# Performance work log

Hardware: AMD Instinct MI355X
Metric: run time of the kernel (lower is better)

## Reference

```python
import jax, jax.numpy as jnp
import numpy as np

EPS = 1e-5

def mean_std_norm(x):
    # instance norm without affine: per-(B,C) mean/std over spatial dims
    mean = jnp.mean(x, axis=(2, 3), keepdims=True)
    var = jnp.var(x, axis=(2, 3), keepdims=True)
    return (x - mean) / jnp.sqrt(var + EPS)

def conv1x1(x, w, b):
    # x: [B,C,H,W], w: [O,C], b: [O]
    return jnp.einsum('oc,bchw->bohw', w, x) + b[None, :, None, None]

def setup_inputs() -> dict:
    key = jax.random.key(0)
    ks = jax.random.split(key, 9)
    C = 512
    s = 1.0 / np.sqrt(C)
    inp = {
        'content_feat': jax.random.normal(ks[0], (4, C, 64, 64), dtype=jnp.float32),
        'f_w': jax.random.normal(ks[1], (C, C), dtype=jnp.float32) * s,
        'f_b': jnp.zeros((C,), dtype=jnp.float32),
        'g_w': jax.random.normal(ks[2], (C, C), dtype=jnp.float32) * s,
        'g_b': jnp.zeros((C,), dtype=jnp.float32),
        'h_w': jax.random.normal(ks[3], (C, C), dtype=jnp.float32) * s,
        'h_b': jnp.zeros((C,), dtype=jnp.float32),
        'o_w': jax.random.normal(ks[4], (C, C), dtype=jnp.float32) * s,
        'o_b': jnp.zeros((C,), dtype=jnp.float32),
    }
    return inp

def reference(content_feat, f_w, f_b, g_w, g_b, h_w, h_b, o_w, o_b):
    B, C, H, W = content_feat.shape
    HW = H * W
    norm = mean_std_norm(content_feat)
    # f(norm) -> [B, HW, C]; g(norm) -> [B, C, HW]
    F_Fc = conv1x1(norm, f_w, f_b).reshape(B, C, HW).transpose(0, 2, 1)
    G_Fs = conv1x1(norm, g_w, g_b).reshape(B, C, HW)
    energy = jnp.einsum('bnc,bcm->bnm', F_Fc, G_Fs)  # [B, HW, HW]
    attention = jax.nn.softmax(energy, axis=-1)
    H_Fs = conv1x1(content_feat, h_w, h_b).reshape(B, C, HW)
    # out = H_Fs @ attention^T : out[b,c,m] = sum_n H_Fs[b,c,n] * att[b,m,n]
    out = jnp.einsum('bcn,bmn->bcm', H_Fs, attention).reshape(B, C, H, W)
    out = conv1x1(out, o_w, o_b)
    return out + content_feat
```

## Files before the change

kernel.cpp:

```cpp
#include <hip/hip_runtime.h>


typedef __bf16 bf16_t;
typedef _Float16 f16_t;
typedef _Float16 f16x8 __attribute__((ext_vector_type(8)));
typedef float f32x4 __attribute__((ext_vector_type(4)));

#define LOG2E 1.44269504088896340736f

__device__ __forceinline__ void gload16(const void* g, void* l) {
  __builtin_amdgcn_global_load_lds(
      (const __attribute__((address_space(1))) void*)g,
      (__attribute__((address_space(3))) void*)l, 16, 0, 0);
}

__global__ void __launch_bounds__(256) stats_k(const float* __restrict__ x,
                                               float* __restrict__ mu,
                                               float* __restrict__ rs) {
  const int bc = blockIdx.x;
  const float4* row = (const float4*)(x + (size_t)bc * 4096);
  float s = 0.f, ss = 0.f;
  for (int i = threadIdx.x; i < 1024; i += 256) {
    float4 v = row[i];
    s += v.x + v.y + v.z + v.w;
    ss += v.x * v.x + v.y * v.y + v.z * v.z + v.w * v.w;
  }
#pragma unroll
  for (int o = 32; o >= 1; o >>= 1) {
    s += __shfl_down(s, o);
    ss += __shfl_down(ss, o);
  }
  __shared__ float as_[4], ass_[4];
  const int w = threadIdx.x >> 6;
  if ((threadIdx.x & 63) == 0) { as_[w] = s; ass_[w] = ss; }
  __syncthreads();
  if (threadIdx.x == 0) {
    float st = as_[0] + as_[1] + as_[2] + as_[3];
    float sst = ass_[0] + ass_[1] + ass_[2] + ass_[3];
    float m = st * (1.f / 4096.f);
    float var = sst * (1.f / 4096.f) - m * m;
    mu[bc] = m;
    rs[bc] = rsqrtf(var + 1e-5f);
  }
}

__global__ void __launch_bounds__(256) wcast2_k(const float* __restrict__ a,
                                                const float* __restrict__ b,
                                                f16_t* __restrict__ dst) {
  const int i = blockIdx.x * 256 + threadIdx.x;
  const int which = i >> 16;
  const int off = i & 65535;
  const float* s = which ? b : a;
  const float4 v = ((const float4*)s)[off];
  alignas(8) f16_t r[4];
  r[0] = (f16_t)v.x; r[1] = (f16_t)v.y; r[2] = (f16_t)v.z; r[3] = (f16_t)v.w;
  *(uint2*)(dst + ((size_t)which << 18) + (size_t)off * 4) = *(const uint2*)r;
}

__global__ void __launch_bounds__(256) mt_k(const float* __restrict__ fw,
                                            const float* __restrict__ gw,
                                            f16_t* __restrict__ Mh) {
  __shared__ float Fs[32][64];
  __shared__ float Gs[32][64];
  const int t = threadIdx.x;
  const int it = blockIdx.x, jt = blockIdx.y;
  float acc[16];
#pragma unroll
  for (int i = 0; i < 16; ++i) acc[i] = 0.f;
  const int jl = t >> 2, ib = (t & 3) * 16;
  const int lr = t >> 4, lc4 = (t & 15) * 4;
  for (int cc = 0; cc < 16; ++cc) {
    __syncthreads();
#pragma unroll
    for (int rep = 0; rep < 2; ++rep) {
      const int r = lr + rep * 16;
      *(float4*)&Fs[r][lc4] = *(const float4*)(fw + (size_t)(cc * 32 + r) * 512 + it * 64 + lc4);
      *(float4*)&Gs[r][lc4] = *(const float4*)(gw + (size_t)(cc * 32 + r) * 512 + jt * 64 + lc4);
    }
    __syncthreads();
#pragma unroll
    for (int c = 0; c < 32; ++c) {
      const float gv = Gs[c][jl];
#pragma unroll
      for (int ii = 0; ii < 16; ++ii) acc[ii] += gv * Fs[c][ib + ii];
    }
  }
  alignas(16) f16_t hi[16];
#pragma unroll
  for (int ii = 0; ii < 16; ++ii) hi[ii] = (f16_t)acc[ii];
  const size_t o = (size_t)(jt * 64 + jl) * 512 + it * 64 + ib;
  *(uint4*)(Mh + o) = *(const uint4*)hi;
  *(uint4*)(Mh + o + 8) = *(const uint4*)(hi + 8);
}

__global__ void __launch_bounds__(256) v_k(const float* __restrict__ gw,
                                           const float* __restrict__ fb,
                                           float* __restrict__ v) {
  const int j = blockIdx.x * 256 + threadIdx.x;
  float s = 0.f;
  for (int c = 0; c < 512; ++c) s += gw[(size_t)c * 512 + j] * fb[c];
  v[j] = s;
}

__global__ void __launch_bounds__(256) u_k(const float* __restrict__ v,
                                           const f16_t* __restrict__ xf,
                                           float* __restrict__ u) {
  const int w = threadIdx.x >> 6, lane = threadIdx.x & 63;
  const int m = blockIdx.x * 4 + w;
  const int b = blockIdx.y;
  const size_t o = ((size_t)b * 4096 + m) * 512 + lane * 8;
  const f16x8 vh = *(const f16x8*)(xf + o);
  const float4 v0 = *(const float4*)(v + lane * 8);
  const float4 v1 = *(const float4*)(v + lane * 8 + 4);
  float s = 0.f;
  const float* vp = &v0.x;
#pragma unroll
  for (int e = 0; e < 4; ++e) s += (float)vh[e] * vp[e];
  const float* vq = &v1.x;
#pragma unroll
  for (int e = 0; e < 4; ++e) s += (float)vh[4 + e] * vq[e];
#pragma unroll
  for (int o2 = 32; o2 >= 1; o2 >>= 1) s += __shfl_down(s, o2);
  if (lane == 0) u[(size_t)b * 4096 + m] = s;
}

__global__ void __launch_bounds__(256) normt_k(const float* __restrict__ x,
                                               const float* __restrict__ mu,
                                               const float* __restrict__ rs,
                                               f16_t* __restrict__ xf,
                                               f16_t* __restrict__ xc) {
  __shared__ float tile[64][65];
  const int t = threadIdx.x;
  const int nt = blockIdx.x, ct = blockIdx.y, b = blockIdx.z;
  const float* src = x + ((size_t)b * 512 + ct * 64) * 4096 + nt * 64;
  {
    const int r = t >> 4, cq = (t & 15) * 4;
#pragma unroll
    for (int it = 0; it < 4; ++it) {
      const int rr = r + it * 16;
      const float4 v = *(const float4*)(src + (size_t)rr * 4096 + cq);
      tile[rr][cq] = v.x; tile[rr][cq + 1] = v.y;
      tile[rr][cq + 2] = v.z; tile[rr][cq + 3] = v.w;
    }
  }
  __syncthreads();
  const int n = t & 63, ch = t >> 6;
  alignas(16) f16_t vf[16], vc[16];
#pragma unroll
  for (int i = 0; i < 16; ++i) {
    const int c = ch * 16 + i;
    const float v = tile[c][n];
    const int gc = b * 512 + ct * 64 + c;
    vc[i] = (f16_t)v;
    vf[i] = (f16_t)((v - mu[gc]) * rs[gc]);
  }
  const size_t o = ((size_t)b * 4096 + nt * 64 + n) * 512 + ct * 64 + ch * 16;
  *(uint4*)(xf + o) = *(const uint4*)vf;
  *(uint4*)(xf + o + 8) = *(const uint4*)(vf + 8);
  *(uint4*)(xc + o) = *(const uint4*)vc;
  *(uint4*)(xc + o + 8) = *(const uint4*)(vc + 8);
}

template <typename OT, int BIAS, bool RESID>
__global__ void __launch_bounds__(256) gemm_k(const f16_t* __restrict__ A,
                                              const f16_t* __restrict__ Bt,
                                              OT* __restrict__ C,
                                              const float* __restrict__ biasM,
                                              const float* __restrict__ biasN,
                                              const float* __restrict__ resid,
                                              long sAb, long sBb, long sCb, int ldC) {
  __shared__ alignas(16) f16_t As[2][128 * 64];
  __shared__ alignas(16) f16_t Bs[2][128 * 64];
  const int t = threadIdx.x;
  const int lane = t & 63;
  const int w = t >> 6;
  const int wr = w >> 1, wc = w & 1;
  const int l15 = lane & 15, lg = lane >> 4;
  const int b = blockIdx.z;
  const int m0 = blockIdx.y * 128, n0 = blockIdx.x * 128;
  const f16_t* Ab = A + (size_t)sAb * b + (size_t)m0 * 512;
  const f16_t* Bb = Bt + (size_t)sBb * b + (size_t)n0 * 512;
  const int srow = t >> 3;
  const int slot = t & 7;

  auto gstage = [&](int pb_, int ks_) {
#pragma unroll
    for (int r_ = 0; r_ < 4; ++r_) {
      const int rr_ = r_ * 32 + srow;
      const size_t go_ = (size_t)rr_ * 512 + ks_ * 64 + ((slot ^ (rr_ & 7)) * 8);
      gload16(Ab + go_, (char*)As[pb_] + r_ * 4096 + w * 1024);
      gload16(Bb + go_, (char*)Bs[pb_] + r_ * 4096 + w * 1024);
    }
  };

  const f32x4 z4 = {0.f, 0.f, 0.f, 0.f};
  f32x4 acc[4][4];
#pragma unroll
  for (int i = 0; i < 4; ++i)
#pragma unroll
    for (int j = 0; j < 4; ++j) acc[i][j] = z4;

  gstage(0, 0);
  __syncthreads();
  for (int ks = 0; ks < 8; ++ks) {
    const int pb = ks & 1;
    if (ks < 7) gstage(pb ^ 1, ks + 1);
#pragma unroll
    for (int kk = 0; kk < 2; ++kk) {
      f16x8 af[4], bfr[4];
#pragma unroll
      for (int i = 0; i < 4; ++i) {
        const int ra = wr * 64 + i * 16 + l15;
        af[i] = *(const f16x8*)((const char*)As[pb] + ra * 128 + (((kk * 4 + lg) ^ (ra & 7)) * 16));
        const int rb = wc * 64 + i * 16 + l15;
        bfr[i] = *(const f16x8*)((const char*)Bs[pb] + rb * 128 + (((kk * 4 + lg) ^ (rb & 7)) * 16));
      }
#pragma unroll
      for (int i = 0; i < 4; ++i)
#pragma unroll
        for (int j = 0; j < 4; ++j)
          acc[i][j] = __builtin_amdgcn_mfma_f32_16x16x32_f16(af[i], bfr[j], acc[i][j], 0, 0, 0);
    }
    __syncthreads();
  }
  OT* Cb = C + (size_t)sCb * b;
#pragma unroll
  for (int i = 0; i < 4; ++i) {
#pragma unroll
    for (int j = 0; j < 4; ++j) {
      const int n = n0 + wc * 64 + j * 16 + l15;
      float bn = 0.f;
      if (BIAS == 2) bn = biasN[n];
#pragma unroll
      for (int r = 0; r < 4; ++r) {
        const int m = m0 + wr * 64 + i * 16 + lg * 4 + r;
        float v = acc[i][j][r] + bn;
        if (BIAS == 1) v += biasM[m];
        if (RESID) v += resid[(size_t)sCb * b + (size_t)m * ldC + n];
        Cb[(size_t)m * ldC + n] = (OT)v;
      }
    }
  }
}

__global__ void __launch_bounds__(512, 1) flash_k(const f16_t* __restrict__ Z,
                                                  const f16_t* __restrict__ X,
                                                  const float* __restrict__ u,
                                                  const f16_t* __restrict__ Hv,
                                                  f16_t* __restrict__ Oat_t) {
  __shared__ alignas(16) f16_t K[2][64 * 256];
  __shared__ alignas(16) f16_t P[64 * 72];
  __shared__ float redm[4][2][16];
  __shared__ float reds[4][2][16];
  __shared__ float alds[64];
  __shared__ float llds[64];

  const int t = threadIdx.x;
  const int lane = t & 63;
  const int w = t >> 6;
  const int wq = w & 3, wk = w >> 2;
  const int l15 = lane & 15, lg = lane >> 4;
  const int bid = blockIdx.x;
  const int xcd = bid & 7;
  const int b = xcd >> 1;
  const int q0 = ((xcd & 1) * 32 + (bid >> 3)) * 64;

  const f16_t* Kb = X + (size_t)b * 4096 * 512;
  const f16_t* Vb = Hv + (size_t)b * 512 * 4096;
  const float* ub = u + (size_t)b * 4096;

  const int srow = w * 2 + (lane >> 5);
  const int slot32 = lane & 31;

  auto stagek = [&](int pb_, int kt_, int hf_) {
    const int k0_ = kt_ * 64;
#pragma unroll
    for (int r_ = 0; r_ < 4; ++r_) {
      const int row_ = r_ * 16 + srow;
      const size_t go_ = (size_t)(k0_ + row_) * 512 + hf_ * 256 + ((slot32 ^ (row_ & 7)) * 8);
      gload16(Kb + go_, (char*)K[pb_] + r_ * 8192 + w * 1024);
    }
  };

#define QKHALF(PB, HF)                                                                        \
  do {                                                                                        \
    _Pragma("unroll") for (int cwl_ = 0; cwl_ < 8; ++cwl_) {                                  \
      const f16x8 qf_ = qf[(HF) * 8 + cwl_];                                                  \
      _Pragma("unroll") for (int mf_ = 0; mf_ < 2; ++mf_) {                                   \
        const int key_ = 32 * wk + 16 * mf_ + l15;                                            \
        const int so_ = ((cwl_ * 4 + lg) ^ (key_ & 7)) * 16;                                  \
        const f16x8 kf_ = *(const f16x8*)((const char*)K[PB] + key_ * 512 + so_);             \
        sacc[mf_] = __builtin_amdgcn_mfma_f32_16x16x32_f16(kf_, qf_, sacc[mf_], 0, 0, 0);     \
      }                                                                                       \
    }                                                                                         \
  } while (0)

  f16x8 qf[16];
  {
    const size_t qo = ((size_t)b * 4096 + q0 + 16 * wq + l15) * 512 + lg * 8;
#pragma unroll
    for (int cw = 0; cw < 16; ++cw) qf[cw] = *(const f16x8*)(Z + qo + cw * 32);
  }
  stagek(0, 0, 0);

  const f32x4 z4 = {0.f, 0.f, 0.f, 0.f};
  f32x4 oacc[4][4];
#pragma unroll
  for (int i = 0; i < 4; ++i)
#pragma unroll
    for (int j = 0; j < 4; ++j) oacc[i][j] = z4;
  float m_run = -3.0e38f, l_run = 0.f;
  const int qrow = 16 * wq + l15;

  __syncthreads();

  for (int kt = 0; kt < 64; ++kt) {
    const int k0 = kt * 64;
    f32x4 sacc[2] = {z4, z4};
    const float4 u0 = *(const float4*)(ub + k0 + 32 * wk + 4 * lg);
    const float4 u1 = *(const float4*)(ub + k0 + 32 * wk + 16 + 4 * lg);
    stagek(1, kt, 1);
    QKHALF(0, 0);
    __syncthreads();
    if (kt < 63) stagek(0, kt + 1, 0);
    f16x8 vpre[4][2];
#pragma unroll
    for (int ct = 0; ct < 4; ++ct) {
      const int c = 64 * w + 16 * ct + l15;
#pragma unroll
      for (int kk = 0; kk < 2; ++kk)
        vpre[ct][kk] = *(const f16x8*)(Vb + (size_t)c * 4096 + k0 + kk * 32 + lg * 8);
    }
    QKHALF(1, 1);
    float pm = -3.0e38f;
    {
      const float* up0 = &u0.x;
      const float* up1 = &u1.x;
#pragma unroll
      for (int j = 0; j < 4; ++j) {
        sacc[0][j] += up0[j];
        sacc[1][j] += up1[j];
        pm = fmaxf(pm, fmaxf(sacc[0][j], sacc[1][j]));
      }
    }
    pm = fmaxf(pm, __shfl_xor(pm, 16));
    pm = fmaxf(pm, __shfl_xor(pm, 32));
    if (lane < 16) redm[wq][wk][lane] = pm;
    __syncthreads();
    const float m_tile = fmaxf(pm, redm[wq][wk ^ 1][l15]);
    float alpha;
    if (m_tile > m_run + 8.f) {
      alpha = exp2f((m_run - m_tile) * LOG2E);
      m_run = m_tile;
    } else {
      alpha = 1.f;
    }
    float ps = 0.f;
    {
      alignas(8) f16_t pk[4];
#pragma unroll
      for (int mf = 0; mf < 2; ++mf) {
#pragma unroll
        for (int j = 0; j < 4; ++j) {
          const float p = exp2f((sacc[mf][j] - m_run) * LOG2E);
          ps += p;
          pk[j] = (f16_t)p;
        }
        *(uint2*)((char*)P + qrow * 144 + 64 * wk + 32 * mf + 8 * lg) = *(const uint2*)pk;
      }
    }
    ps += __shfl_xor(ps, 16);
    ps += __shfl_xor(ps, 32);
    if (lane < 16) {
      reds[wq][wk][lane] = ps;
      if (wk == 0) alds[16 * wq + lane] = alpha;
    }
    __syncthreads();
    const float s_tile = reds[wq][0][l15] + reds[wq][1][l15];
    l_run = l_run * alpha + s_tile;
    float aq[4];
#pragma unroll
    for (int qt = 0; qt < 4; ++qt) aq[qt] = alds[16 * qt + l15];
    const bool need = (aq[0] != 1.f) || (aq[1] != 1.f) || (aq[2] != 1.f) || (aq[3] != 1.f);
    if (__any(need)) {
#pragma unroll
      for (int ct = 0; ct < 4; ++ct)
#pragma unroll
        for (int qt = 0; qt < 4; ++qt) oacc[ct][qt] *= aq[qt];
    }
#pragma unroll
    for (int kk = 0; kk < 2; ++kk) {
      f16x8 bp[4];
#pragma unroll
      for (int qt = 0; qt < 4; ++qt) {
        const int q = 16 * qt + l15;
        bp[qt] = *(const f16x8*)((const char*)P + q * 144 + kk * 64 + lg * 16);
      }
#pragma unroll
      for (int ct = 0; ct < 4; ++ct)
#pragma unroll
        for (int qt = 0; qt < 4; ++qt)
          oacc[ct][qt] =
              __builtin_amdgcn_mfma_f32_16x16x32_f16(vpre[ct][kk], bp[qt], oacc[ct][qt], 0, 0, 0);
    }
  }
#undef QKHALF
  if (wk == 0 && lane < 16) llds[16 * wq + lane] = l_run;
  __syncthreads();
  float inv[4];
#pragma unroll
  for (int qt = 0; qt < 4; ++qt) inv[qt] = 1.f / llds[16 * qt + l15];
#pragma unroll
  for (int ct = 0; ct < 4; ++ct)
#pragma unroll
    for (int qt = 0; qt < 4; ++qt) {
      alignas(8) f16_t o4[4];
#pragma unroll
      for (int j = 0; j < 4; ++j) o4[j] = (f16_t)(oacc[ct][qt][j] * inv[qt]);
      *(uint2*)(Oat_t + ((size_t)b * 4096 + q0 + 16 * qt + l15) * 512 + 64 * w + 16 * ct + 4 * lg) =
          *(const uint2*)o4;
    }
}

extern "C" void kernel_launch(void* const* d_in, const int* in_sizes, int n_in,
                              void* d_out, int out_size, void* d_ws, size_t ws_size,
                              hipStream_t stream) {
  const float* x = (const float*)d_in[0];
  const float* fw = (const float*)d_in[1];
  const float* fb = (const float*)d_in[2];
  const float* gw = (const float*)d_in[3];
  const float* gb = (const float*)d_in[4];
  const float* hw = (const float*)d_in[5];
  const float* hb = (const float*)d_in[6];
  const float* ow = (const float*)d_in[7];
  const float* ob = (const float*)d_in[8];
  float* out = (float*)d_out;
  (void)gb;

  const size_t BIG = (size_t)4 * 4096 * 512 * sizeof(f16_t);
  char* p = (char*)d_ws;
  float* mu = (float*)p; p += 2048 * sizeof(float);
  float* rs = (float*)p; p += 2048 * sizeof(float);
  float* vv = (float*)p; p += 512 * sizeof(float);
  float* uu = (float*)p; p += (size_t)4 * 4096 * sizeof(float);
  f16_t* w2 = (f16_t*)p; p += (size_t)2 * 512 * 512 * sizeof(f16_t);
  f16_t* Mh = (f16_t*)p; p += (size_t)512 * 512 * sizeof(f16_t);
  f16_t* xf = (f16_t*)p; p += BIG;
  f16_t* xc = (f16_t*)p; p += BIG;
  f16_t* Zf = (f16_t*)p; p += BIG;
  f16_t* Hv = (f16_t*)p; p += BIG;
  f16_t* Oat_t = xc;

  f16_t* whb = w2;
  f16_t* wob = w2 + 262144;

  const long sD = (long)4096 * 512;

  stats_k<<<2048, 256, 0, stream>>>(x, mu, rs);
  wcast2_k<<<512, 256, 0, stream>>>(hw, ow, w2);
  mt_k<<<dim3(8, 8), 256, 0, stream>>>(fw, gw, Mh);
  v_k<<<2, 256, 0, stream>>>(gw, fb, vv);
  normt_k<<<dim3(64, 8, 4), 256, 0, stream>>>(x, mu, rs, xf, xc);
  u_k<<<dim3(1024, 4), 256, 0, stream>>>(vv, xf, uu);
  gemm_k<f16_t, 0, false><<<dim3(4, 32, 4), 256, 0, stream>>>(
      xf, Mh, Zf, nullptr, nullptr, nullptr, sD, 0, sD, 512);
  gemm_k<f16_t, 1, false><<<dim3(32, 4, 4), 256, 0, stream>>>(
      whb, xc, Hv, hb, nullptr, nullptr, 0, sD, sD, 4096);
  flash_k<<<256, 512, 0, stream>>>(Zf, xf, uu, Hv, Oat_t);
  gemm_k<float, 1, true><<<dim3(32, 4, 4), 256, 0, stream>>>(
      wob, Oat_t, out, ob, nullptr, x, 0, sD, sD, 4096);

  (void)in_sizes; (void)n_in; (void)out_size; (void)ws_size;
}
```

Measured before the change: 373.4 us.

## Process two key tiles per softmax step and split QK accumulators

The flash attention loop now handles 128 keys per iteration: two 64-key tiles of QK^T are computed before a single max/sum reduction and rescale. This halves the softmax reduction and barrier overhead per key. The QK MFMA chain is also split into even and odd accumulators to shorten dependency chains. The P buffer is widened to 128 columns, and register pressure rises from holding two V prefetch sets and four score tiles.

```diff
diff --git a/kernel.cpp b/kernel.cpp
--- a/kernel.cpp
+++ b/kernel.cpp
@@ -249,7 +249,7 @@
                                                   const f16_t* __restrict__ Hv,
                                                   f16_t* __restrict__ Oat_t) {
   __shared__ alignas(16) f16_t K[2][64 * 256];
-  __shared__ alignas(16) f16_t P[64 * 72];
+  __shared__ alignas(16) f16_t P[64 * 136];
   __shared__ float redm[4][2][16];
   __shared__ float reds[4][2][16];
   __shared__ float alds[64];
@@ -282,17 +282,27 @@
     }
   };
 
-#define QKHALF(PB, HF)                                                                        \
+#define QKHALF(PB, HF, S0, S1)                                                                \
   do {                                                                                        \
+    f32x4 p0 = z4, p1 = z4, p2 = z4, p3 = z4;                                                 \
     _Pragma("unroll") for (int cwl_ = 0; cwl_ < 8; ++cwl_) {                                  \
       const f16x8 qf_ = qf[(HF) * 8 + cwl_];                                                  \
-      _Pragma("unroll") for (int mf_ = 0; mf_ < 2; ++mf_) {                                   \
-        const int key_ = 32 * wk + 16 * mf_ + l15;                                            \
-        const int so_ = ((cwl_ * 4 + lg) ^ (key_ & 7)) * 16;                                  \
-        const f16x8 kf_ = *(const f16x8*)((const char*)K[PB] + key_ * 512 + so_);             \
-        sacc[mf_] = __builtin_amdgcn_mfma_f32_16x16x32_f16(kf_, qf_, sacc[mf_], 0, 0, 0);     \
+      const int key0_ = 32 * wk + l15;                                                        \
+      const int key1_ = 32 * wk + 16 + l15;                                                   \
+      const f16x8 kf0_ = *(const f16x8*)((const char*)K[PB] + key0_ * 512 +                   \
+                                         (((cwl_ * 4 + lg) ^ (key0_ & 7)) * 16));             \
+      const f16x8 kf1_ = *(const f16x8*)((const char*)K[PB] + key1_ * 512 +                   \
+                                         (((cwl_ * 4 + lg) ^ (key1_ & 7)) * 16));             \
+      if (cwl_ & 1) {                                                                         \
+        p1 = __builtin_amdgcn_mfma_f32_16x16x32_f16(kf0_, qf_, p1, 0, 0, 0);                  \
+        p3 = __builtin_amdgcn_mfma_f32_16x16x32_f16(kf1_, qf_, p3, 0, 0, 0);                  \
+      } else {                                                                                \
+        p0 = __builtin_amdgcn_mfma_f32_16x16x32_f16(kf0_, qf_, p0, 0, 0, 0);                  \
+        p2 = __builtin_amdgcn_mfma_f32_16x16x32_f16(kf1_, qf_, p2, 0, 0, 0);                  \
       }                                                                                       \
     }                                                                                         \
+    S0 += p0 + p1;                                                                            \
+    S1 += p2 + p3;                                                                            \
   } while (0)
 
   f16x8 qf[16];
@@ -314,33 +324,46 @@
 
   __syncthreads();
 
-  for (int kt = 0; kt < 64; ++kt) {
-    const int k0 = kt * 64;
-    f32x4 sacc[2] = {z4, z4};
+  for (int bt = 0; bt < 32; ++bt) {
+    const int ktA = 2 * bt, ktB = 2 * bt + 1;
+    const int k0 = bt * 128;
+    f32x4 sA0 = z4, sA1 = z4, sB0 = z4, sB1 = z4;
     const float4 u0 = *(const float4*)(ub + k0 + 32 * wk + 4 * lg);
     const float4 u1 = *(const float4*)(ub + k0 + 32 * wk + 16 + 4 * lg);
-    stagek(1, kt, 1);
-    QKHALF(0, 0);
-    __syncthreads();
-    if (kt < 63) stagek(0, kt + 1, 0);
-    f16x8 vpre[4][2];
+    const float4 u2 = *(const float4*)(ub + k0 + 64 + 32 * wk + 4 * lg);
+    const float4 u3 = *(const float4*)(ub + k0 + 64 + 32 * wk + 16 + 4 * lg);
+    stagek(1, ktA, 1);
+    QKHALF(0, 0, sA0, sA1);
+    __syncthreads();
+    stagek(0, ktB, 0);
+    QKHALF(1, 1, sA0, sA1);
+    __syncthreads();
+    stagek(1, ktB, 1);
+    f16x8 vpreA[4][2];
 #pragma unroll
     for (int ct = 0; ct < 4; ++ct) {
       const int c = 64 * w + 16 * ct + l15;
 #pragma unroll
       for (int kk = 0; kk < 2; ++kk)
-        vpre[ct][kk] = *(const f16x8*)(Vb + (size_t)c * 4096 + k0 + kk * 32 + lg * 8);
-    }
-    QKHALF(1, 1);
+        vpreA[ct][kk] = *(const f16x8*)(Vb + (size_t)c * 4096 + k0 + kk * 32 + lg * 8);
+    }
+    QKHALF(0, 0, sB0, sB1);
+    __syncthreads();
+    stagek(0, (ktA + 2) & 63, 0);
+    QKHALF(1, 1, sB0, sB1);
     float pm = -3.0e38f;
     {
       const float* up0 = &u0.x;
       const float* up1 = &u1.x;
+      const float* up2 = &u2.x;
+      const float* up3 = &u3.x;
 #pragma unroll
       for (int j = 0; j < 4; ++j) {
-        sacc[0][j] += up0[j];
-        sacc[1][j] += up1[j];
-        pm = fmaxf(pm, fmaxf(sacc[0][j], sacc[1][j]));
+        sA0[j] += up0[j];
+        sA1[j] += up1[j];
+        sB0[j] += up2[j];
+        sB1[j] += up3[j];
+        pm = fmaxf(pm, fmaxf(fmaxf(sA0[j], sA1[j]), fmaxf(sB0[j], sB1[j])));
       }
     }
     pm = fmaxf(pm, __shfl_xor(pm, 16));
@@ -358,15 +381,17 @@
     float ps = 0.f;
     {
       alignas(8) f16_t pk[4];
-#pragma unroll
-      for (int mf = 0; mf < 2; ++mf) {
+      f32x4* sp[4] = {&sA0, &sA1, &sB0, &sB1};
+#pragma unroll
+      for (int sfi = 0; sfi < 4; ++sfi) {
+        const int byo = qrow * 272 + (sfi >> 1) * 128 + 64 * wk + 32 * (sfi & 1) + 8 * lg;
 #pragma unroll
         for (int j = 0; j < 4; ++j) {
-          const float p = exp2f((sacc[mf][j] - m_run) * LOG2E);
+          const float p = exp2f(((*sp[sfi])[j] - m_run) * LOG2E);
           ps += p;
           pk[j] = (f16_t)p;
         }
-        *(uint2*)((char*)P + qrow * 144 + 64 * wk + 32 * mf + 8 * lg) = *(const uint2*)pk;
+        *(uint2*)((char*)P + byo) = *(const uint2*)pk;
       }
     }
     ps += __shfl_xor(ps, 16);
@@ -388,20 +413,43 @@
 #pragma unroll
         for (int qt = 0; qt < 4; ++qt) oacc[ct][qt] *= aq[qt];
     }
+    f16x8 vpreB[4][2];
+#pragma unroll
+    for (int ct = 0; ct < 4; ++ct) {
+      const int c = 64 * w + 16 * ct + l15;
+#pragma unroll
+      for (int kk = 0; kk < 2; ++kk)
+        vpreB[ct][kk] = *(const f16x8*)(Vb + (size_t)c * 4096 + k0 + 64 + kk * 32 + lg * 8);
+    }
 #pragma unroll
     for (int kk = 0; kk < 2; ++kk) {
       f16x8 bp[4];
 #pragma unroll
       for (int qt = 0; qt < 4; ++qt) {
         const int q = 16 * qt + l15;
-        bp[qt] = *(const f16x8*)((const char*)P + q * 144 + kk * 64 + lg * 16);
+        bp[qt] = *(const f16x8*)((const char*)P + q * 272 + kk * 64 + lg * 16);
       }
 #pragma unroll
       for (int ct = 0; ct < 4; ++ct)
 #pragma unroll
         for (int qt = 0; qt < 4; ++qt)
           oacc[ct][qt] =
-              __builtin_amdgcn_mfma_f32_16x16x32_f16(vpre[ct][kk], bp[qt], oacc[ct][qt], 0, 0, 0);
+              __builtin_amdgcn_mfma_f32_16x16x32_f16(vpreA[ct][kk], bp[qt], oacc[ct][qt], 0, 0, 0);
+    }
+#pragma unroll
+    for (int kk = 0; kk < 2; ++kk) {
+      f16x8 bp[4];
+#pragma unroll
+      for (int qt = 0; qt < 4; ++qt) {
+        const int q = 16 * qt + l15;
+        bp[qt] = *(const f16x8*)((const char*)P + q * 272 + 128 + kk * 64 + lg * 16);
+      }
+#pragma unroll
+      for (int ct = 0; ct < 4; ++ct)
+#pragma unroll
+        for (int qt = 0; qt < 4; ++qt)
+          oacc[ct][qt] =
+              __builtin_amdgcn_mfma_f32_16x16x32_f16(vpreB[ct][kk], bp[qt], oacc[ct][qt], 0, 0, 0);
     }
   }
 #undef QKHALF
```

Result: slower. 452.0 us (+21.1%).

## Fold h-projection into output projection via precomputed Wo·Wh product

Applied to the files above, without the earlier changes.

Because the attention-weighted sum is linear, the value projection h is folded into the output projection. A new kernel precomputes Wo·Wh as fp16, and a folded bias Wo·hb+ob is computed separately. The flash kernel then consumes the raw fp16 input (cast inside the stats kernel) instead of a projected H, which removes one full GEMM over the activations. The cost is an extra small 512x512 fp32 matmul and a change in rounding, since the combined weight is rounded to fp16 once.

```diff
diff --git a/kernel.cpp b/kernel.cpp
--- a/kernel.cpp
+++ b/kernel.cpp
@@ -16,14 +16,19 @@
 
 __global__ void __launch_bounds__(256) stats_k(const float* __restrict__ x,
                                                float* __restrict__ mu,
-                                               float* __restrict__ rs) {
+                                               float* __restrict__ rs,
+                                               f16_t* __restrict__ xv) {
   const int bc = blockIdx.x;
   const float4* row = (const float4*)(x + (size_t)bc * 4096);
+  f16_t* vrow = xv + (size_t)bc * 4096;
   float s = 0.f, ss = 0.f;
   for (int i = threadIdx.x; i < 1024; i += 256) {
     float4 v = row[i];
     s += v.x + v.y + v.z + v.w;
     ss += v.x * v.x + v.y * v.y + v.z * v.z + v.w * v.w;
+    alignas(8) f16_t h[4];
+    h[0] = (f16_t)v.x; h[1] = (f16_t)v.y; h[2] = (f16_t)v.z; h[3] = (f16_t)v.w;
+    *(uint2*)(vrow + i * 4) = *(const uint2*)h;
   }
 #pragma unroll
   for (int o = 32; o >= 1; o >>= 1) {
@@ -44,19 +49,6 @@
   }
 }
 
-__global__ void __launch_bounds__(256) wcast2_k(const float* __restrict__ a,
-                                                const float* __restrict__ b,
-                                                f16_t* __restrict__ dst) {
-  const int i = blockIdx.x * 256 + threadIdx.x;
-  const int which = i >> 16;
-  const int off = i & 65535;
-  const float* s = which ? b : a;
-  const float4 v = ((const float4*)s)[off];
-  alignas(8) f16_t r[4];
-  r[0] = (f16_t)v.x; r[1] = (f16_t)v.y; r[2] = (f16_t)v.z; r[3] = (f16_t)v.w;
-  *(uint2*)(dst + ((size_t)which << 18) + (size_t)off * 4) = *(const uint2*)r;
-}
-
 __global__ void __launch_bounds__(256) mt_k(const float* __restrict__ fw,
                                             const float* __restrict__ gw,
                                             f16_t* __restrict__ Mh) {
@@ -93,6 +85,48 @@
   *(uint4*)(Mh + o + 8) = *(const uint4*)(hi + 8);
 }
 
+__global__ void __launch_bounds__(256) mt2_k(const float* __restrict__ hw,
+                                             const float* __restrict__ ow,
+                                             f16_t* __restrict__ Wf) {
+  __shared__ float Fs[32][64];
+  __shared__ float Os[64][33];
+  const int t = threadIdx.x;
+  const int it = blockIdx.x, jt = blockIdx.y;
+  float acc[16];
+#pragma unroll
+  for (int i = 0; i < 16; ++i) acc[i] = 0.f;
+  const int jl = t >> 2, ib = (t & 3) * 16;
+  const int lr = t >> 4, lc4 = (t & 15) * 4;
+  const int oj = t >> 2, ok = (t & 3) * 8;
+  for (int kc = 0; kc < 16; ++kc) {
+    __syncthreads();
+#pragma unroll
+    for (int rep = 0; rep < 2; ++rep) {
+      const int r = lr + rep * 16;
+      *(float4*)&Fs[r][lc4] = *(const float4*)(hw + (size_t)(kc * 32 + r) * 512 + it * 64 + lc4);
+    }
+    {
+      const float4 a = *(const float4*)(ow + (size_t)(jt * 64 + oj) * 512 + kc * 32 + ok);
+      const float4 bq = *(const float4*)(ow + (size_t)(jt * 64 + oj) * 512 + kc * 32 + ok + 4);
+      Os[oj][ok] = a.x; Os[oj][ok + 1] = a.y; Os[oj][ok + 2] = a.z; Os[oj][ok + 3] = a.w;
+      Os[oj][ok + 4] = bq.x; Os[oj][ok + 5] = bq.y; Os[oj][ok + 6] = bq.z; Os[oj][ok + 7] = bq.w;
+    }
+    __syncthreads();
+#pragma unroll
+    for (int k = 0; k < 32; ++k) {
+      const float gv = Os[jl][k];
+#pragma unroll
+      for (int ii = 0; ii < 16; ++ii) acc[ii] += gv * Fs[k][ib + ii];
+    }
+  }
+  alignas(16) f16_t hi[16];
+#pragma unroll
+  for (int ii = 0; ii < 16; ++ii) hi[ii] = (f16_t)acc[ii];
+  const size_t o = (size_t)(jt * 64 + jl) * 512 + it * 64 + ib;
+  *(uint4*)(Wf + o) = *(const uint4*)hi;
+  *(uint4*)(Wf + o + 8) = *(const uint4*)(hi + 8);
+}
+
 __global__ void __launch_bounds__(256) v_k(const float* __restrict__ gw,
                                            const float* __restrict__ fb,
                                            float* __restrict__ v) {
@@ -100,6 +134,23 @@
   float s = 0.f;
   for (int c = 0; c < 512; ++c) s += gw[(size_t)c * 512 + j] * fb[c];
   v[j] = s;
+}
+
+__global__ void __launch_bounds__(256) bias2_k(const float* __restrict__ ow,
+                                               const float* __restrict__ hb,
+                                               const float* __restrict__ ob,
+                                               float* __restrict__ b2) {
+  const int w = threadIdx.x >> 6, lane = threadIdx.x & 63;
+  const int j = blockIdx.x * 4 + w;
+  const float4 a = *(const float4*)(ow + (size_t)j * 512 + lane * 8);
+  const float4 b = *(const float4*)(ow + (size_t)j * 512 + lane * 8 + 4);
+  const float4 h0 = *(const float4*)(hb + lane * 8);
+  const float4 h1 = *(const float4*)(hb + lane * 8 + 4);
+  float s = a.x * h0.x + a.y * h0.y + a.z * h0.z + a.w * h0.w +
+            b.x * h1.x + b.y * h1.y + b.z * h1.z + b.w * h1.w;
+#pragma unroll
+  for (int o2 = 32; o2 >= 1; o2 >>= 1) s += __shfl_down(s, o2);
+  if (lane == 0) b2[j] = s + ob[j];
 }
 
 __global__ void __launch_bounds__(256) u_k(const float* __restrict__ v,
@@ -127,8 +178,7 @@
 __global__ void __launch_bounds__(256) normt_k(const float* __restrict__ x,
                                                const float* __restrict__ mu,
                                                const float* __restrict__ rs,
-                                               f16_t* __restrict__ xf,
-                                               f16_t* __restrict__ xc) {
+                                               f16_t* __restrict__ xf) {
   __shared__ float tile[64][65];
   const int t = threadIdx.x;
   const int nt = blockIdx.x, ct = blockIdx.y, b = blockIdx.z;
@@ -145,20 +195,17 @@
   }
   __syncthreads();
   const int n = t & 63, ch = t >> 6;
-  alignas(16) f16_t vf[16], vc[16];
+  alignas(16) f16_t vf[16];
 #pragma unroll
   for (int i = 0; i < 16; ++i) {
     const int c = ch * 16 + i;
     const float v = tile[c][n];
     const int gc = b * 512 + ct * 64 + c;
-    vc[i] = (f16_t)v;
     vf[i] = (f16_t)((v - mu[gc]) * rs[gc]);
   }
   const size_t o = ((size_t)b * 4096 + nt * 64 + n) * 512 + ct * 64 + ch * 16;
   *(uint4*)(xf + o) = *(const uint4*)vf;
   *(uint4*)(xf + o + 8) = *(const uint4*)(vf + 8);
-  *(uint4*)(xc + o) = *(const uint4*)vc;
-  *(uint4*)(xc + o + 8) = *(const uint4*)(vc + 8);
 }
 
 template <typename OT, int BIAS, bool RESID>
@@ -442,33 +489,29 @@
   float* mu = (float*)p; p += 2048 * sizeof(float);
   float* rs = (float*)p; p += 2048 * sizeof(float);
   float* vv = (float*)p; p += 512 * sizeof(float);
+  float* b2 = (float*)p; p += 512 * sizeof(float);
   float* uu = (float*)p; p += (size_t)4 * 4096 * sizeof(float);
-  f16_t* w2 = (f16_t*)p; p += (size_t)2 * 512 * 512 * sizeof(f16_t);
   f16_t* Mh = (f16_t*)p; p += (size_t)512 * 512 * sizeof(f16_t);
+  f16_t* Wf = (f16_t*)p; p += (size_t)512 * 512 * sizeof(f16_t);
   f16_t* xf = (f16_t*)p; p += BIG;
-  f16_t* xc = (f16_t*)p; p += BIG;
+  f16_t* xv = (f16_t*)p; p += BIG;
   f16_t* Zf = (f16_t*)p; p += BIG;
-  f16_t* Hv = (f16_t*)p; p += BIG;
-  f16_t* Oat_t = xc;
-
-  f16_t* whb = w2;
-  f16_t* wob = w2 + 262144;
+  f16_t* Oat_t = (f16_t*)p; p += BIG;
 
   const long sD = (long)4096 * 512;
 
-  stats_k<<<2048, 256, 0, stream>>>(x, mu, rs);
-  wcast2_k<<<512, 256, 0, stream>>>(hw, ow, w2);
+  stats_k<<<2048, 256, 0, stream>>>(x, mu, rs, xv);
   mt_k<<<dim3(8, 8), 256, 0, stream>>>(fw, gw, Mh);
+  mt2_k<<<dim3(8, 8), 256, 0, stream>>>(hw, ow, Wf);
   v_k<<<2, 256, 0, stream>>>(gw, fb, vv);
-  normt_k<<<dim3(64, 8, 4), 256, 0, stream>>>(x, mu, rs, xf, xc);
+  bias2_k<<<128, 256, 0, stream>>>(ow, hb, ob, b2);
+  normt_k<<<dim3(64, 8, 4), 256, 0, stream>>>(x, mu, rs, xf);
   u_k<<<dim3(1024, 4), 256, 0, stream>>>(vv, xf, uu);
   gemm_k<f16_t, 0, false><<<dim3(4, 32, 4), 256, 0, stream>>>(
       xf, Mh, Zf, nullptr, nullptr, nullptr, sD, 0, sD, 512);
-  gemm_k<f16_t, 1, false><<<dim3(32, 4, 4), 256, 0, stream>>>(
-      whb, xc, Hv, hb, nullptr, nullptr, 0, sD, sD, 4096);
-  flash_k<<<256, 512, 0, stream>>>(Zf, xf, uu, Hv, Oat_t);
+  flash_k<<<256, 512, 0, stream>>>(Zf, xf, uu, xv, Oat_t);
   gemm_k<float, 1, true><<<dim3(32, 4, 4), 256, 0, stream>>>(
-      wob, Oat_t, out, ob, nullptr, x, 0, sD, sD, 4096);
+      Wf, Oat_t, out, b2, nullptr, x, 0, sD, sD, 4096);
 
   (void)in_sizes; (void)n_in; (void)out_size; (void)ws_size;
 }
```

New measurement: 389.7 us. +4.4%, slower.
